# Kernel optimization log

Hardware: AMD Instinct MI355X
Metric: run time of the kernel (lower is better)

The kernel has to match this reference:

```python
import jax, jax.numpy as jnp
import numpy as np
from jax import lax

PART = 224   # PART_IMAGE_SIZE
PAD = 224    # PAD_SIZE
TOPN = 4
IOU_THRESH = 0.25
N_ANCHORS = 1614


def _conv(x, w, b, stride, pad):
    y = lax.conv_general_dilated(x, w, (stride, stride), [(pad, pad), (pad, pad)],
                                 dimension_numbers=('NCHW', 'OIHW', 'NCHW'))
    return y + b[None, :, None, None]


def _iou(box, boxes):
    # box [4], boxes [N,4] as (y0,x0,y1,x1)
    yy0 = jnp.maximum(box[0], boxes[:, 0]); xx0 = jnp.maximum(box[1], boxes[:, 1])
    yy1 = jnp.minimum(box[2], boxes[:, 2]); xx1 = jnp.minimum(box[3], boxes[:, 3])
    inter = jnp.clip(yy1 - yy0, 0.0) * jnp.clip(xx1 - xx0, 0.0)
    a = (box[2] - box[0]) * (box[3] - box[1])
    areas = (boxes[:, 2] - boxes[:, 0]) * (boxes[:, 3] - boxes[:, 1])
    return inter / (a + areas - inter)


def _nms(scores, boxes):
    # hard NMS keeping TOPN boxes; returns indices [TOPN]
    valid = jnp.ones(scores.shape, dtype=bool)
    idxs = []
    for _ in range(TOPN):
        i = jnp.argmax(jnp.where(valid, scores, -jnp.inf))
        idxs.append(i)
        valid = valid & (_iou(boxes[i], boxes) <= IOU_THRESH)
    return jnp.stack(idxs)


def _crop_resize(img, box):
    # img [3,Hp,Wp] padded image, box [4] float; bilinear, align_corners=True,
    # matching F.interpolate(x_pad[:, :, y0:y1, x0:x1], (PART, PART))
    Hp, Wp = img.shape[1], img.shape[2]
    def coords(c0, c1, L):
        t = jnp.arange(PART, dtype=img.dtype) / (PART - 1)
        c = c0 + (c1 - 1.0 - c0) * t          # absolute source coordinate
        cf = jnp.floor(c)
        lo = jnp.clip(cf.astype(jnp.int32), 0, L - 1)
        hi = jnp.clip(lo + 1, 0, L - 1)
        return lo, hi, c - cf
    yl, yh, wy = coords(box[0], box[2], Hp)
    xl, xh, wx = coords(box[1], box[3], Wp)
    g = lambda yi, xi: img[:, yi[:, None], xi[None, :]]   # [3,PART,PART]
    return ((1 - wy)[:, None] * ((1 - wx) * g(yl, xl) + wx * g(yl, xh))
            + wy[:, None] * ((1 - wx) * g(yh, xl) + wx * g(yh, xh)))


def setup_inputs() -> dict:
    key = jax.random.key(0)
    ks = jax.random.split(key, 20)
    x = jax.random.uniform(ks[0], (16, 3, 448, 448), dtype=jnp.float32)
    rpn_feature = jax.random.normal(ks[1], (16, 2048, 14, 14), dtype=jnp.float32)
    # valid boxes inside the padded 896x896 image
    y0 = jax.random.randint(ks[2], (N_ANCHORS,), 0, 560)
    x0 = jax.random.randint(ks[3], (N_ANCHORS,), 0, 560)
    h = jax.random.randint(ks[4], (N_ANCHORS,), 32, 336)
    w = jax.random.randint(ks[5], (N_ANCHORS,), 32, 336)
    anchors = jnp.stack([y0, x0, jnp.minimum(y0 + h, 896), jnp.minimum(x0 + w, 896)], axis=1).astype(jnp.int32)
    s = 0.02
    inp = {
        'x': x, 'rpn_feature': rpn_feature, 'anchors': anchors,
        'w_down1': jax.random.normal(ks[6], (128, 2048, 3, 3), jnp.float32) * s,
        'b_down1': jnp.zeros((128,), jnp.float32),
        'w_down2': jax.random.normal(ks[7], (128, 128, 3, 3), jnp.float32) * s,
        'b_down2': jnp.zeros((128,), jnp.float32),
        'w_down3': jax.random.normal(ks[8], (128, 128, 3, 3), jnp.float32) * s,
        'b_down3': jnp.zeros((128,), jnp.float32),
        'w_tidy1': jax.random.normal(ks[9], (6, 128, 1, 1), jnp.float32) * s,
        'b_tidy1': jnp.zeros((6,), jnp.float32),
        'w_tidy2': jax.random.normal(ks[10], (6, 128, 1, 1), jnp.float32) * s,
        'b_tidy2': jnp.zeros((6,), jnp.float32),
        'w_tidy3': jax.random.normal(ks[11], (9, 128, 1, 1), jnp.float32) * s,
        'b_tidy3': jnp.zeros((9,), jnp.float32),
    }
    return inp


def reference(x, rpn_feature, anchors,
              w_down1, b_down1, w_down2, b_down2, w_down3, b_down3,
              w_tidy1, b_tidy1, w_tidy2, b_tidy2, w_tidy3, b_tidy3):
    B = x.shape[0]
    # ProposalNet
    d1 = jax.nn.relu(_conv(rpn_feature, w_down1, b_down1, 1, 1))   # [B,128,14,14]
    d2 = jax.nn.relu(_conv(d1, w_down2, b_down2, 2, 1))            # [B,128,7,7]
    d3 = jax.nn.relu(_conv(d2, w_down3, b_down3, 2, 1))            # [B,128,4,4]
    t1 = _conv(d1, w_tidy1, b_tidy1, 1, 0).reshape(B, -1)
    t2 = _conv(d2, w_tidy2, b_tidy2, 1, 0).reshape(B, -1)
    t3 = _conv(d3, w_tidy3, b_tidy3, 1, 0).reshape(B, -1)
    rpn_score = jnp.concatenate([t1, t2, t3], axis=1)              # [B, 1614]
    boxes = anchors.astype(x.dtype)                                # [N,4]
    top_n_index = jax.vmap(lambda s: _nms(s, boxes))(rpn_score)    # [B,TOPN]
    top_n_prob = jnp.take_along_axis(rpn_score, top_n_index, axis=1)
    x_pad = jnp.pad(x, ((0, 0), (0, 0), (PAD, PAD), (PAD, PAD)))   # [B,3,896,896]
    sel_boxes = boxes[top_n_index]                                 # [B,TOPN,4]
    part_imgs = jax.vmap(lambda img, bxs: jax.vmap(lambda b: _crop_resize(img, b))(bxs))(x_pad, sel_boxes)
    # part_imgs: [B,TOPN,3,PART,PART]
    return rpn_score, top_n_index, top_n_prob, part_imgs
```

## Files before the change

### kernel.cpp

```cpp
#include <hip/hip_runtime.h>
#include <hip/hip_bf16.h>

#define NB 16
#define NA 1614
#define NBP (NB * 196 * 128)
#define NBP2 (NB * 128 * 49)

typedef __bf16 bf16x8 __attribute__((ext_vector_type(8)));
typedef float f32x4 __attribute__((ext_vector_type(4)));

__device__ __forceinline__ unsigned short f2bf(float v) {
  unsigned u = __float_as_uint(v);
  unsigned r = (u + 0x7FFFu + ((u >> 16) & 1u)) >> 16;
  return (unsigned short)r;
}
__device__ __forceinline__ float bf2f(unsigned short s) {
  return __uint_as_float(((unsigned)s) << 16);
}

__global__ __launch_bounds__(256)
void prep(const float* __restrict__ w, const float* __restrict__ in,
          unsigned short* __restrict__ wTh, unsigned short* __restrict__ wTl,
          unsigned short* __restrict__ aTh, unsigned short* __restrict__ aTl) {
  __shared__ float sbuf[32 * 289];
  const int bid = blockIdx.x;
  if (bid < 1024) {
    const int chunk = bid & 63, b = bid >> 6;
    const float* src = in + ((size_t)b * 2048 + chunk * 32) * 196;
#pragma unroll
    for (int r = 0; r < 7; r++) {
      int e = threadIdx.x + 256 * r;
      if (e < 1568) {
        int ic = e / 49, f = e - ic * 49;
        float4 v = ((const float4*)(src + (size_t)ic * 196))[f];
        float* d = sbuf + ic * 201 + f * 4;
        d[0] = v.x; d[1] = v.y; d[2] = v.z; d[3] = v.w;
      }
    }
    __syncthreads();
    unsigned short* oh = aTh + (size_t)bid * (196 * 32);
    unsigned short* ol = aTl + (size_t)bid * (196 * 32);
#pragma unroll
    for (int r = 0; r < 4; r++) {
      int e = threadIdx.x + 256 * r;
      if (e < 784) {
        int pos = e >> 2, part = e & 3;
        unsigned short hv[8], lv[8];
#pragma unroll
        for (int j = 0; j < 8; j++) {
          float v = sbuf[(part * 8 + j) * 201 + pos];
          unsigned short h = f2bf(v);
          hv[j] = h;
          lv[j] = f2bf(v - bf2f(h));
        }
        ((uint4*)oh)[e] = *(uint4*)hv;
        ((uint4*)ol)[e] = *(uint4*)lv;
      }
    }
  } else {
    const int bid2 = bid - 1024;
    const int ocg = bid2 & 3, ks = (bid2 >> 2) & 3, kcp = bid2 >> 4;
    const int oc0 = ocg * 32;
    const int ic0 = kcp * 128 + ks * 32;
#pragma unroll
    for (int r = 0; r < 9; r++) {
      int f = threadIdx.x + 256 * r;
      int o = f / 72, rem4 = f - o * 72;
      float4 v = *(const float4*)(w + ((size_t)(oc0 + o) * 2048 + ic0) * 9 + rem4 * 4);
      float* d = sbuf + o * 289 + rem4 * 4;
      d[0] = v.x; d[1] = v.y; d[2] = v.z; d[3] = v.w;
    }
    __syncthreads();
#pragma unroll
    for (int r = 0; r < 36; r++) {
      int e = threadIdx.x + 256 * r;
      int tap = e >> 10, rem = e & 1023;
      int o = rem >> 5, ic = rem & 31;
      float v = sbuf[o * 289 + ic * 9 + tap];
      unsigned short h = f2bf(v);
      size_t g2 = ((size_t)(kcp * 36 + tap * 4 + ks) << 12) + oc0 * 32 + rem;
      wTh[g2] = h;
      wTl[g2] = f2bf(v - bf2f(h));
    }
  }
}

#define APL 1360
#define ABUF (4 * APL)

#define LOADB(H, L, T, K)                                                     \
  {                                                                           \
    const size_t o_ = ((size_t)(kc * 36 + (T) * 4 + (K)) << 12) + bln;        \
    const unsigned short* ph_ = wTh + o_;                                     \
    const unsigned short* pq_ = wTl + o_;                                     \
    H[0] = *(const bf16x8*)(ph_);                                             \
    H[1] = *(const bf16x8*)(ph_ + 512);                                       \
    L[0] = *(const bf16x8*)(pq_);                                             \
    L[1] = *(const bf16x8*)(pq_ + 512);                                       \
  }

#define STEP(IT, BUH, BUL, BNH, BNL)                                          \
  {                                                                           \
    const int it_ = (IT);                                                     \
    const int ks_ = it_ / 9, tap_ = it_ - ks_ * 9;                            \
    {             \
      const int ni_ = (it_ < 35) ? it_ + 1 : 35;                              \
      const int nk_ = ni_ / 9, nt_ = ni_ - nk_ * 9;                           \
      LOADB(BNH, BNL, nt_, nk_);                                              \
    }                                                                         \
    if (ks_ < 3) {        \
      if (tap_ == 3 || tap_ == 4) {                                           \
        int e_ = tid + 256 * (tap_ - 3);                                      \
        if (e_ < ne) {                                                        \
          int u_ = pos04 + e_;                                                \
          int pos_ = u_ >> 2, part_ = u_ & 3;                                 \
          int py_ = pos_ / 14, px_ = pos_ - py_ * 14;                         \
          int d_ = (((ks_ + 1) & 1) ? ABUF : 0) + part_ * APL                 \
                   + (py_ + 1 - rowoff) * 136 + (px_ + 1) * 8;                \
          *(uint4*)(sAh + d_) = sgh;                                          \
          *(uint4*)(sAl + d_) = sgl;                                          \
        }                                                                     \
      }                                                                       \
      if (tap_ == 2 || tap_ == 3) {                                           \
        const uint4* gh_ = (const uint4*)(aTh + ((size_t)(b * 64 + kc * 4 + ks_ + 1) * 196) * 32); \
        const uint4* gl_ = (const uint4*)(aTl + ((size_t)(b * 64 + kc * 4 + ks_ + 1) * 196) * 32); \
        int e_ = tid + 256 * (tap_ - 2);                                      \
        if (e_ < ne) { sgh = gh_[pos04 + e_]; sgl = gl_[pos04 + e_]; }        \
      }                                                                       \
    }                                                                         \
    const int t8_ = (tap_ / 3) * 136 + (tap_ - (tap_ / 3) * 3) * 8;           \
    const unsigned short* pah_ = sAh + (ks_ & 1) * ABUF + qoff + t8_;         \
    const unsigned short* pal_ = sAl + (ks_ & 1) * ABUF + qoff + t8_;         \
    bf16x8 afh[7], afl[7];                                                    \
    _Pragma("unroll") for (int mf = 0; mf < 7; mf++) {                        \
      afh[mf] = *(const bf16x8*)(pah_ + abase[mf]);                           \
      afl[mf] = *(const bf16x8*)(pal_ + abase[mf]);                           \
    }                                                                         \
    _Pragma("unroll") for (int mf = 0; mf < 7; mf++)                          \
      _Pragma("unroll") for (int nf = 0; nf < 2; nf++)                        \
        acc[mf][nf] = __builtin_amdgcn_mfma_f32_16x16x32_bf16(afh[mf], BUH[nf], acc[mf][nf], 0, 0, 0); \
    _Pragma("unroll") for (int mf = 0; mf < 7; mf++)                          \
      _Pragma("unroll") for (int nf = 0; nf < 2; nf++)                        \
        acc[mf][nf] = __builtin_amdgcn_mfma_f32_16x16x32_bf16(afl[mf], BUH[nf], acc[mf][nf], 0, 0, 0); \
    _Pragma("unroll") for (int mf = 0; mf < 7; mf++)                          \
      _Pragma("unroll") for (int nf = 0; nf < 2; nf++)                        \
        acc[mf][nf] = __builtin_amdgcn_mfma_f32_16x16x32_bf16(afh[mf], BUL[nf], acc[mf][nf], 0, 0, 0); \
    if (tap_ == 8) __syncthreads();                                           \
  }

__global__ __launch_bounds__(256, 2)
void conv1_mfma(const unsigned short* __restrict__ aTh, const unsigned short* __restrict__ aTl,
                const unsigned short* __restrict__ wTh, const unsigned short* __restrict__ wTl,
                float* __restrict__ p1) {
  const int bid = blockIdx.x;
  const int kc = bid & 15;
  const int b  = (bid >> 4) & 15;
  const int mh = bid >> 8;
  const int tid = threadIdx.x;
  const int wid = tid >> 6, lane = tid & 63;
  const int wn = wid;
  const int q = lane >> 4, ln = lane & 15;

  __shared__ unsigned short sAh[2 * ABUF];
  __shared__ unsigned short sAl[2 * ABUF];

  const int rowoff = 6 * mh;
  const int pos0 = mh ? 98 : 0;
  const int ne   = mh ? 392 : 504;
  const int pos04 = pos0 * 4;

  for (int e = tid; e < 2 * ABUF / 2; e += 256) {
    ((unsigned int*)sAh)[e] = 0u;
    ((unsigned int*)sAl)[e] = 0u;
  }

  int abase[7];
#pragma unroll
  for (int mf = 0; mf < 7; mf++) {
    int row = mh * 112 + mf * 16 + ln;
    int y = row / 14, x = row - y * 14;
    abase[mf] = (row < 196) ? ((y - rowoff) * 136 + x * 8) : 0;
  }
  const int qoff = q * APL;
  const int bln = (wn * 32 + ln) * 32 + q * 8;

  f32x4 acc[7][2];
#pragma unroll
  for (int mf = 0; mf < 7; mf++)
#pragma unroll
    for (int nf = 0; nf < 2; nf++) acc[mf][nf] = (f32x4){0.f, 0.f, 0.f, 0.f};

  uint4 sgh = {}, sgl = {};

  __syncthreads();

  {
    const uint4* gh = (const uint4*)(aTh + ((size_t)(b * 64 + kc * 4) * 196) * 32);
    const uint4* gl = (const uint4*)(aTl + ((size_t)(b * 64 + kc * 4) * 196) * 32);
#pragma unroll
    for (int r = 0; r < 2; r++) {
      int e = tid + 256 * r;
      if (e < ne) {
        int u = pos04 + e;
        int pos = u >> 2, part = u & 3;
        int py = pos / 14, px = pos - py * 14;
        int d = part * APL + (py + 1 - rowoff) * 136 + (px + 1) * 8;
        *(uint4*)(sAh + d) = gh[u];
        *(uint4*)(sAl + d) = gl[u];
      }
    }
  }
  bf16x8 b0h[2], b0l[2], b1h[2], b1l[2];
  LOADB(b0h, b0l, 0, 0);
  __syncthreads();

  for (int it = 0; it < 36; it += 2) {
    STEP(it,     b0h, b0l, b1h, b1l);
    STEP(it + 1, b1h, b1l, b0h, b0l);
  }

  float* pk = p1 + ((size_t)kc * NB + b) * 196 * 128;
#pragma unroll
  for (int mf = 0; mf < 7; mf++) {
    const int row0 = mh * 112 + mf * 16 + q * 4;
#pragma unroll
    for (int nf = 0; nf < 2; nf++) {
      const int oc = wn * 32 + nf * 16 + ln;
#pragma unroll
      for (int r = 0; r < 4; r++) {
        const int row = row0 + r;
        if (row < 196) pk[(size_t)row * 128 + oc] = acc[mf][nf][r];
      }
    }
  }
}

__global__ __launch_bounds__(256)
void conv1_finish_p(const float* __restrict__ p1, const float* __restrict__ bias,
                    float* __restrict__ d1) {
  __shared__ float s[28 * 132];
  const int bid = blockIdx.x;
  const int pt = bid % 7, b = bid / 7;
  const int tid = threadIdx.x;
#pragma unroll
  for (int r = 0; r < 4; r++) {
    int u = tid + 256 * r;
    if (u < 896) {
      int pos = u >> 5, oc4 = u & 31;
      const float* base = p1 + ((size_t)(b * 196 + pt * 28 + pos)) * 128 + oc4 * 4;
      float4 sum = ((const float4*)bias)[oc4];
#pragma unroll
      for (int k = 0; k < 16; k++) {
        float4 v = *(const float4*)(base + (size_t)k * NBP);
        sum.x += v.x; sum.y += v.y; sum.z += v.z; sum.w += v.w;
      }
      sum.x = fmaxf(sum.x, 0.f); sum.y = fmaxf(sum.y, 0.f);
      sum.z = fmaxf(sum.z, 0.f); sum.w = fmaxf(sum.w, 0.f);
      *(float4*)(s + pos * 132 + oc4 * 4) = sum;
    }
  }
  __syncthreads();
#pragma unroll
  for (int r = 0; r < 4; r++) {
    int u = tid + 256 * r;
    if (u < 896) {
      int oc = u / 7, f = u - oc * 7;
      float4 v;
      v.x = s[(f * 4 + 0) * 132 + oc];
      v.y = s[(f * 4 + 1) * 132 + oc];
      v.z = s[(f * 4 + 2) * 132 + oc];
      v.w = s[(f * 4 + 3) * 132 + oc];
      *(float4*)(d1 + ((size_t)b * 128 + oc) * 196 + pt * 28 + f * 4) = v;
    }
  }
}

__global__ void conv2_part(const float* __restrict__ d1, const float* __restrict__ w,
                           float* __restrict__ p2) {
  const int bid = blockIdx.x;
  const int kc = bid & 3, oct = (bid >> 2) & 3, b = bid >> 4;
  const int ic0 = kc * 32, oc0 = oct * 32;
  const int tid = threadIdx.x;
  const int icg = tid >> 6;
  const int ocq = (tid >> 3) & 7;
  const int rw  = tid & 7;

  __shared__ float s_in[32 * 320];
  __shared__ float s_w[32 * 324];

#pragma unroll
  for (int r = 0; r < 32; r++) {
    const int e = tid + 256 * r;
    const int ch = e >> 8, idx = e & 255;
    const int tr = idx >> 4, tc = idx & 15;
    const int iy = tr - 1, ix = tc - 1;
    float v = 0.f;
    if ((unsigned)iy < 14u && (unsigned)ix < 14u)
      v = d1[((size_t)b * 128 + ic0 + ch) * 196 + iy * 14 + ix];
    s_in[ch * 320 + tr * 20 + tc] = v;
  }
#pragma unroll
  for (int r = 0; r < 36; r++) {
    const int e = tid + 256 * r;
    const int oc = e / 288, rem = e - oc * 288;
    const int ch = rem / 9, tap = rem - ch * 9;
    s_w[ch * 324 + tap * 36 + oc] =
        w[(size_t)(oc0 + oc) * 1152 + (size_t)ic0 * 9 + rem];
  }
  __syncthreads();

  float acc[4][7];
#pragma unroll
  for (int oc = 0; oc < 4; oc++)
#pragma unroll
    for (int x = 0; x < 7; x++) acc[oc][x] = 0.f;

  if (rw < 7) {
    for (int ic = 0; ic < 8; ic++) {
      const int ci = icg * 8 + ic;
      const float* irow = s_in + ci * 320;
      const float* wq = s_w + ci * 324 + ocq * 4;
#pragma unroll
      for (int ky = 0; ky < 3; ky++) {
        const float* r = irow + (2 * rw + ky) * 20;
        const float4 f0 = *(const float4*)(r);
        const float4 f1 = *(const float4*)(r + 4);
        const float4 f2 = *(const float4*)(r + 8);
        const float4 f3 = *(const float4*)(r + 12);
        const float ev[8] = {f0.x, f0.z, f1.x, f1.z, f2.x, f2.z, f3.x, f3.z};
        const float od[7] = {f0.y, f0.w, f1.y, f1.w, f2.y, f2.w, f3.y};
        const float4 w0 = *(const float4*)(wq + (ky * 3 + 0) * 36);
        const float4 w1 = *(const float4*)(wq + (ky * 3 + 1) * 36);
        const float4 w2 = *(const float4*)(wq + (ky * 3 + 2) * 36);
        const float w0a[4] = {w0.x, w0.y, w0.z, w0.w};
        const float w1a[4] = {w1.x, w1.y, w1.z, w1.w};
        const float w2a[4] = {w2.x, w2.y, w2.z, w2.w};
#pragma unroll
        for (int oc = 0; oc < 4; oc++) {
          const float a0 = w0a[oc], a1 = w1a[oc], a2 = w2a[oc];
#pragma unroll
          for (int x = 0; x < 7; x++)
            acc[oc][x] = fmaf(a0, ev[x], fmaf(a1, od[x], fmaf(a2, ev[x + 1], acc[oc][x])));
        }
      }
    }
  }
  __syncthreads();

  if (icg > 0 && rw < 7) {
    float* dst = s_w + ((icg - 1) * 56 + ocq * 7 + rw) * 28;
#pragma unroll
    for (int oc = 0; oc < 4; oc++)
#pragma unroll
      for (int x = 0; x < 7; x++) dst[oc * 7 + x] = acc[oc][x];
  }
  __syncthreads();
  if (icg == 0 && rw < 7) {
#pragma unroll
    for (int g = 0; g < 3; g++) {
      const float* src = s_w + (g * 56 + ocq * 7 + rw) * 28;
#pragma unroll
      for (int oc = 0; oc < 4; oc++)
#pragma unroll
        for (int x = 0; x < 7; x++) acc[oc][x] += src[oc * 7 + x];
    }
    float* po = p2 + (((size_t)kc * NB + b) * 128 + oc0 + ocq * 4) * 49 + rw * 7;
#pragma unroll
    for (int oc = 0; oc < 4; oc++)
#pragma unroll
      for (int x = 0; x < 7; x++) po[oc * 49 + x] = acc[oc][x];
  }
}

__global__ void conv3_part(const float* __restrict__ p2, const float* __restrict__ bd2,
                           const float* __restrict__ w, float* __restrict__ p3) {
  const int bid = blockIdx.x;
  const int kc = bid & 1, oct = (bid >> 1) & 7, b = bid >> 4;
  const int ic0 = kc * 64, oc0 = oct * 16;
  const int tid = threadIdx.x;
  const int oc = tid >> 4, p = tid & 15;
  const int y = p >> 2, x = p & 3;

  __shared__ float s_in[64 * 108];
  __shared__ float s_w[64 * 144];

#pragma unroll
  for (int r = 0; r < 21; r++) {
    const int e = tid + 256 * r;
    if (e < 64 * 81) {
      const int ch = e / 81, idx = e - ch * 81;
      const int tr = idx / 9, tc = idx - tr * 9;
      const int iy = tr - 1, ix = tc - 1;
      float v = 0.f;
      if ((unsigned)iy < 7u && (unsigned)ix < 7u) {
        const size_t ii = ((size_t)b * 128 + ic0 + ch) * 49 + iy * 7 + ix;
        v = bd2[ic0 + ch] + p2[ii];
        v += p2[(size_t)NBP2 + ii];
        v += p2[(size_t)2 * NBP2 + ii];
        v += p2[(size_t)3 * NBP2 + ii];
        v = fmaxf(v, 0.f);
      }
      s_in[ch * 108 + tr * 12 + tc] = v;
    }
  }
#pragma unroll
  for (int r = 0; r < 36; r++) {
    const int e = tid + 256 * r;
    const int o = e / 576, rem = e - o * 576;
    const int ch = rem / 9, tap = rem - ch * 9;
    s_w[ch * 144 + tap * 16 + o] =
        w[(size_t)(oc0 + o) * 1152 + (size_t)ic0 * 9 + rem];
  }
  __syncthreads();

  float acc = 0.f;
  for (int ic = 0; ic < 64; ic++) {
    const float* wrow = s_w + ic * 144 + oc;
    const float* irow = s_in + ic * 108 + 2 * y * 12 + 2 * x;
#pragma unroll
    for (int ky = 0; ky < 3; ky++)
#pragma unroll
      for (int kx = 0; kx < 3; kx++)
        acc = fmaf(wrow[(ky * 3 + kx) * 16], irow[ky * 12 + kx], acc);
  }
  p3[(((size_t)kc * NB + b) * 128 + oc0 + oc) * 16 + p] = acc;
}

__global__ __launch_bounds__(256, 1)
void score_nms(const float* __restrict__ d1,
               const float* __restrict__ p2, const float* __restrict__ bd2,
               const float* __restrict__ p3, const float* __restrict__ bd3,
               const float* __restrict__ w1, const float* __restrict__ b1,
               const float* __restrict__ w2, const float* __restrict__ b2,
               const float* __restrict__ w3, const float* __restrict__ b3,
               const int* __restrict__ anchors, float* __restrict__ score,
               float* __restrict__ out_idx, float* __restrict__ out_prob,
               float* __restrict__ sel) {
  __shared__ float s_in[32 * 200];
  __shared__ float s_w[21 * 128];
  __shared__ float s_b[21];
  __shared__ float s_sc[NA];
  __shared__ float s_bx[NA * 4];
  __shared__ float r_s[256];
  __shared__ int r_i[256];
  const int b = blockIdx.x, tid = threadIdx.x;

  for (int i = tid; i < 768; i += 256) s_w[i] = w1[i];
  for (int i = tid; i < 768; i += 256) s_w[768 + i] = w2[i];
  for (int i = tid; i < 1152; i += 256) s_w[1536 + i] = w3[i];
  if (tid < 21) s_b[tid] = (tid < 6) ? b1[tid] : (tid < 12) ? b2[tid - 6] : b3[tid - 12];
  for (int i = tid; i < NA; i += 256) {
    s_bx[i * 4 + 0] = (float)anchors[i * 4 + 0];
    s_bx[i * 4 + 1] = (float)anchors[i * 4 + 1];
    s_bx[i * 4 + 2] = (float)anchors[i * 4 + 2];
    s_bx[i * 4 + 3] = (float)anchors[i * 4 + 3];
  }

  float acc[5] = {0.f, 0.f, 0.f, 0.f, 0.f};
  for (int chunk = 0; chunk < 4; chunk++) {
    __syncthreads();
    const float* src = d1 + ((size_t)b * 128 + chunk * 32) * 196;
#pragma unroll
    for (int r = 0; r < 7; r++) {
      int e = tid + 256 * r;
      if (e < 1568) {
        int ic = e / 49, f = e - ic * 49;
        *(float4*)(s_in + ic * 200 + f * 4) = ((const float4*)(src + (size_t)ic * 196))[f];
      }
    }
    __syncthreads();
#pragma unroll
    for (int k = 0; k < 5; k++) {
      int j = tid + 256 * k;
      if (j < 1176) {
        int oc = j / 196, p = j - oc * 196;
        const float* wr = s_w + oc * 128 + chunk * 32;
        float s = acc[k];
#pragma unroll
        for (int ic = 0; ic < 32; ic++) s = fmaf(wr[ic], s_in[ic * 200 + p], s);
        acc[k] = s;
      }
    }
  }
#pragma unroll
  for (int k = 0; k < 5; k++) {
    int j = tid + 256 * k;
    if (j < 1176) {
      int oc = j / 196;
      float s = acc[k] + s_b[oc];
      s_sc[j] = s;
      score[b * NA + j] = s;
    }
  }

  __syncthreads();
  {
    const size_t base = (size_t)b * 6272;
#pragma unroll
    for (int r = 0; r < 7; r++) {
      int e = tid + 256 * r;
      if (e < 1568) {
        const float4 v0 = *(const float4*)(p2 + base + e * 4);
        const float4 v1 = *(const float4*)(p2 + (size_t)NBP2 + base + e * 4);
        const float4 v2 = *(const float4*)(p2 + (size_t)2 * NBP2 + base + e * 4);
        const float4 v3 = *(const float4*)(p2 + (size_t)3 * NBP2 + base + e * 4);
        const float s0[4] = {v0.x, v0.y, v0.z, v0.w};
        const float s1[4] = {v1.x, v1.y, v1.z, v1.w};
        const float s2[4] = {v2.x, v2.y, v2.z, v2.w};
        const float s3[4] = {v3.x, v3.y, v3.z, v3.w};
        float o[4];
#pragma unroll
        for (int k = 0; k < 4; k++) {
          const int oc = (e * 4 + k) / 49;
          float s = bd2[oc] + s0[k];
          s += s1[k]; s += s2[k]; s += s3[k];
          o[k] = fmaxf(s, 0.f);
        }
        float4 vv; vv.x = o[0]; vv.y = o[1]; vv.z = o[2]; vv.w = o[3];
        *(float4*)(s_in + e * 4) = vv;
      }
    }
  }
  __syncthreads();
#pragma unroll
  for (int k = 0; k < 2; k++) {
    int jj = tid + 256 * k;
    if (jj < 294) {
      int oc = jj / 49, p = jj - oc * 49;
      const float* wr = s_w + 768 + oc * 128;
      float s = s_b[6 + oc];
#pragma unroll 8
      for (int ic = 0; ic < 128; ic++) s = fmaf(wr[ic], s_in[ic * 49 + p], s);
      s_sc[1176 + jj] = s;
      score[b * NA + 1176 + jj] = s;
    }
  }

  __syncthreads();
  {
    const float4* s0 = (const float4*)(p3 + (size_t)b * 2048);
    const float4* s1 = (const float4*)(p3 + 32768 + (size_t)b * 2048);
#pragma unroll
    for (int r = 0; r < 2; r++) {
      int e = tid + 256 * r;
      if (e < 512) {
        float4 a = s0[e], c = s1[e];
        float bb = bd3[e >> 2];
        float4 v;
        v.x = fmaxf(a.x + c.x + bb, 0.f);
        v.y = fmaxf(a.y + c.y + bb, 0.f);
        v.z = fmaxf(a.z + c.z + bb, 0.f);
        v.w = fmaxf(a.w + c.w + bb, 0.f);
        *(float4*)(s_in + e * 4) = v;
      }
    }
  }
  __syncthreads();
  if (tid < 144) {
    int oc = tid >> 4, p = tid & 15;
    const float* wr = s_w + 1536 + oc * 128;
    float s = s_b[12 + oc];
#pragma unroll 8
    for (int ic = 0; ic < 128; ic++) s = fmaf(wr[ic], s_in[ic * 16 + p], s);
    s_sc[1470 + tid] = s;
    score[b * NA + 1470 + tid] = s;
  }
  __syncthreads();

  for (int t = 0; t < 4; t++) {
    float bs = -__builtin_inff();
    int bi = NA;
    for (int i = tid; i < NA; i += 256) {
      float s = s_sc[i];
      if (s > bs || (s == bs && i < bi)) { bs = s; bi = i; }
    }
    r_s[tid] = bs; r_i[tid] = bi;
    __syncthreads();
    for (int off = 128; off > 0; off >>= 1) {
      if (tid < off) {
        float s2 = r_s[tid + off]; int i2 = r_i[tid + off];
        if (s2 > r_s[tid] || (s2 == r_s[tid] && i2 < r_i[tid])) { r_s[tid] = s2; r_i[tid] = i2; }
      }
      __syncthreads();
    }
    const int idx = r_i[0];
    const float by0 = s_bx[idx * 4 + 0], bx0 = s_bx[idx * 4 + 1];
    const float by1 = s_bx[idx * 4 + 2], bx1 = s_bx[idx * 4 + 3];
    if (tid == 0) {
      out_idx[b * 4 + t] = (float)idx;
      out_prob[b * 4 + t] = s_sc[idx];
      sel[(b * 4 + t) * 4 + 0] = by0;
      sel[(b * 4 + t) * 4 + 1] = bx0;
      sel[(b * 4 + t) * 4 + 2] = by1;
      sel[(b * 4 + t) * 4 + 3] = bx1;
    }
    __syncthreads();
    const float a = (by1 - by0) * (bx1 - bx0);
    for (int i = tid; i < NA; i += 256) {
      float cy0 = s_bx[i * 4 + 0], cx0 = s_bx[i * 4 + 1];
      float cy1 = s_bx[i * 4 + 2], cx1 = s_bx[i * 4 + 3];
      float yy0 = fmaxf(by0, cy0), xx0 = fmaxf(bx0, cx0);
      float yy1 = fminf(by1, cy1), xx1 = fminf(bx1, cx1);
      float inter = fmaxf(yy1 - yy0, 0.f) * fmaxf(xx1 - xx0, 0.f);
      float ar = (cy1 - cy0) * (cx1 - cx0);
      float iou = inter / (a + ar - inter);
      if (iou > 0.25f) s_sc[i] = -__builtin_inff();
    }
    __syncthreads();
  }
}

__global__ void crop_kernel(const float* __restrict__ x, const float* __restrict__ sel,
                            float* __restrict__ out) {
  int i4 = blockIdx.x * 256 + threadIdx.x;
  const int total4 = NB * 4 * 3 * 224 * 56;
  if (i4 >= total4) return;
  int px0 = (i4 % 56) * 4;
  int t = i4 / 56;
  int py = t % 224; t /= 224;
  int ch = t % 3;  t /= 3;
  int n  = t % 4;
  int b  = t / 4;

  const float* bx = sel + (b * 4 + n) * 4;
  const float y0 = bx[0], x0 = bx[1], y1 = bx[2], x1 = bx[3];

  float ty = (float)py / 223.0f;
  float cy = y0 + (y1 - 1.0f - y0) * ty;
  float cyf = floorf(cy);
  int ylo = (int)cyf; ylo = ylo < 0 ? 0 : (ylo > 895 ? 895 : ylo);
  int yhi = ylo + 1 > 895 ? 895 : ylo + 1;
  float wy = cy - cyf;

  const float* img = x + ((size_t)b * 3 + ch) * 448 * 448;
  auto g = [&](int yy, int xx) -> float {
    yy -= 224; xx -= 224;
    if ((unsigned)yy < 448u && (unsigned)xx < 448u)
      return img[(size_t)yy * 448 + xx];
    return 0.f;
  };

  float4 res;
  float* rp = &res.x;
#pragma unroll
  for (int k = 0; k < 4; k++) {
    float tx = (float)(px0 + k) / 223.0f;
    float cx = x0 + (x1 - 1.0f - x0) * tx;
    float cxf = floorf(cx);
    int xlo = (int)cxf; xlo = xlo < 0 ? 0 : (xlo > 895 ? 895 : xlo);
    int xhi = xlo + 1 > 895 ? 895 : xlo + 1;
    float wx = cx - cxf;
    float v00 = g(ylo, xlo), v01 = g(ylo, xhi);
    float v10 = g(yhi, xlo), v11 = g(yhi, xhi);
    rp[k] = (1.f - wy) * ((1.f - wx) * v00 + wx * v01) +
            wy * ((1.f - wx) * v10 + wx * v11);
  }
  *(float4*)(out + (size_t)i4 * 4) = res;
}

extern "C" void kernel_launch(void* const* d_in, const int* in_sizes, int n_in,
                              void* d_out, int out_size, void* d_ws, size_t ws_size,
                              hipStream_t stream) {
  const float* x    = (const float*)d_in[0];
  const float* rpn  = (const float*)d_in[1];
  const int*   anc  = (const int*)d_in[2];
  const float* w_d1 = (const float*)d_in[3];
  const float* b_d1 = (const float*)d_in[4];
  const float* w_d2 = (const float*)d_in[5];
  const float* b_d2 = (const float*)d_in[6];
  const float* w_d3 = (const float*)d_in[7];
  const float* b_d3 = (const float*)d_in[8];
  const float* w_t1 = (const float*)d_in[9];
  const float* b_t1 = (const float*)d_in[10];
  const float* w_t2 = (const float*)d_in[11];
  const float* b_t2 = (const float*)d_in[12];
  const float* w_t3 = (const float*)d_in[13];
  const float* b_t3 = (const float*)d_in[14];

  float* out = (float*)d_out;
  float* ws = (float*)d_ws;

  float* d1  = ws;
  float* d2  = d1 + 401408;
  float* d3  = d2 + 100352;
  float* sel = d3 + 32768;
  float* p2  = sel + 256;
  float* p3  = p2 + 401408;
  unsigned short* wTh = (unsigned short*)(p3 + 65536);
  unsigned short* wTl = wTh + 2359296;
  unsigned short* aTh = wTl + 2359296;
  unsigned short* aTl = aTh + 6422528;

  float* score    = out;
  float* out_idx  = out + 25824;
  float* out_prob = out + 25888;
  float* parts    = out + 25952;
  float* p1       = parts;

  prep<<<dim3(1280), dim3(256), 0, stream>>>(w_d1, rpn, wTh, wTl, aTh, aTl);
  conv1_mfma<<<dim3(512), dim3(256), 0, stream>>>(aTh, aTl, wTh, wTl, p1);
  conv1_finish_p<<<dim3(112), dim3(256), 0, stream>>>(p1, b_d1, d1);
  conv2_part<<<dim3(256), dim3(256), 0, stream>>>(d1, w_d2, p2);
  conv3_part<<<dim3(256), dim3(256), 0, stream>>>(p2, b_d2, w_d3, p3);
  score_nms<<<dim3(16), dim3(256), 0, stream>>>(d1, p2, b_d2, p3, b_d3, w_t1, b_t1, w_t2, b_t2,
                                                w_t3, b_t3, anc, score, out_idx, out_prob, sel);
  crop_kernel<<<dim3(9408), dim3(256), 0, stream>>>(x, sel, parts);
}
```

Baseline: 277.5 us.

## Split conv1 finish into more blocks and drop conv2 in-block channel reduction

conv1_finish_p now handles 7 positions per block across 448 blocks instead of 28 positions across 112, so more CUs share the 16-way partial-sum reduction. Its output stores become scalar rather than float4. conv2_part now gives each thread one output channel across all 32 input channels, rather than 4 channels over a quarter of the inputs followed by a shared-memory cross-group reduction. This removes two syncthreads and the reduction pass, but each thread runs a longer serial loop with fewer weight reuses per input load.

```diff
diff --git a/kernel.cpp b/kernel.cpp
--- a/kernel.cpp
+++ b/kernel.cpp
@@ -238,39 +238,30 @@
 __global__ __launch_bounds__(256)
 void conv1_finish_p(const float* __restrict__ p1, const float* __restrict__ bias,
                     float* __restrict__ d1) {
-  __shared__ float s[28 * 132];
+  __shared__ float s[7 * 132];
   const int bid = blockIdx.x;
-  const int pt = bid % 7, b = bid / 7;
+  const int pt = bid % 28, b = bid / 28;
   const int tid = threadIdx.x;
+  if (tid < 224) {
+    int pos = tid >> 5, oc4 = tid & 31;
+    const float* base = p1 + ((size_t)(b * 196 + pt * 7 + pos)) * 128 + oc4 * 4;
+    float4 sum = ((const float4*)bias)[oc4];
+#pragma unroll
+    for (int k = 0; k < 16; k++) {
+      float4 v = *(const float4*)(base + (size_t)k * NBP);
+      sum.x += v.x; sum.y += v.y; sum.z += v.z; sum.w += v.w;
+    }
+    sum.x = fmaxf(sum.x, 0.f); sum.y = fmaxf(sum.y, 0.f);
+    sum.z = fmaxf(sum.z, 0.f); sum.w = fmaxf(sum.w, 0.f);
+    *(float4*)(s + pos * 132 + oc4 * 4) = sum;
+  }
+  __syncthreads();
 #pragma unroll
   for (int r = 0; r < 4; r++) {
-    int u = tid + 256 * r;
-    if (u < 896) {
-      int pos = u >> 5, oc4 = u & 31;
-      const float* base = p1 + ((size_t)(b * 196 + pt * 28 + pos)) * 128 + oc4 * 4;
-      float4 sum = ((const float4*)bias)[oc4];
-#pragma unroll
-      for (int k = 0; k < 16; k++) {
-        float4 v = *(const float4*)(base + (size_t)k * NBP);
-        sum.x += v.x; sum.y += v.y; sum.z += v.z; sum.w += v.w;
-      }
-      sum.x = fmaxf(sum.x, 0.f); sum.y = fmaxf(sum.y, 0.f);
-      sum.z = fmaxf(sum.z, 0.f); sum.w = fmaxf(sum.w, 0.f);
-      *(float4*)(s + pos * 132 + oc4 * 4) = sum;
-    }
-  }
-  __syncthreads();
-#pragma unroll
-  for (int r = 0; r < 4; r++) {
-    int u = tid + 256 * r;
-    if (u < 896) {
-      int oc = u / 7, f = u - oc * 7;
-      float4 v;
-      v.x = s[(f * 4 + 0) * 132 + oc];
-      v.y = s[(f * 4 + 1) * 132 + oc];
-      v.z = s[(f * 4 + 2) * 132 + oc];
-      v.w = s[(f * 4 + 3) * 132 + oc];
-      *(float4*)(d1 + ((size_t)b * 128 + oc) * 196 + pt * 28 + f * 4) = v;
+    int e = tid + 256 * r;
+    if (e < 896) {
+      int oc = e / 7, f = e - oc * 7;
+      d1[((size_t)b * 128 + oc) * 196 + pt * 7 + f] = s[f * 132 + oc];
     }
   }
 }
@@ -281,9 +272,7 @@
   const int kc = bid & 3, oct = (bid >> 2) & 3, b = bid >> 4;
   const int ic0 = kc * 32, oc0 = oct * 32;
   const int tid = threadIdx.x;
-  const int icg = tid >> 6;
-  const int ocq = (tid >> 3) & 7;
-  const int rw  = tid & 7;
+  const int ocl = tid >> 3, rw = tid & 7;
 
   __shared__ float s_in[32 * 320];
   __shared__ float s_w[32 * 324];
@@ -309,17 +298,11 @@
   }
   __syncthreads();
 
-  float acc[4][7];
-#pragma unroll
-  for (int oc = 0; oc < 4; oc++)
-#pragma unroll
-    for (int x = 0; x < 7; x++) acc[oc][x] = 0.f;
-
   if (rw < 7) {
-    for (int ic = 0; ic < 8; ic++) {
-      const int ci = icg * 8 + ic;
-      const float* irow = s_in + ci * 320;
-      const float* wq = s_w + ci * 324 + ocq * 4;
+    float acc[7] = {};
+    for (int ic = 0; ic < 32; ic++) {
+      const float* wrow = s_w + ic * 324 + ocl;
+      const float* irow = s_in + ic * 320;
 #pragma unroll
       for (int ky = 0; ky < 3; ky++) {
         const float* r = irow + (2 * rw + ky) * 20;
@@ -329,46 +312,17 @@
         const float4 f3 = *(const float4*)(r + 12);
         const float ev[8] = {f0.x, f0.z, f1.x, f1.z, f2.x, f2.z, f3.x, f3.z};
         const float od[7] = {f0.y, f0.w, f1.y, f1.w, f2.y, f2.w, f3.y};
-        const float4 w0 = *(const float4*)(wq + (ky * 3 + 0) * 36);
-        const float4 w1 = *(const float4*)(wq + (ky * 3 + 1) * 36);
-        const float4 w2 = *(const float4*)(wq + (ky * 3 + 2) * 36);
-        const float w0a[4] = {w0.x, w0.y, w0.z, w0.w};
-        const float w1a[4] = {w1.x, w1.y, w1.z, w1.w};
-        const float w2a[4] = {w2.x, w2.y, w2.z, w2.w};
-#pragma unroll
-        for (int oc = 0; oc < 4; oc++) {
-          const float a0 = w0a[oc], a1 = w1a[oc], a2 = w2a[oc];
-#pragma unroll
-          for (int x = 0; x < 7; x++)
-            acc[oc][x] = fmaf(a0, ev[x], fmaf(a1, od[x], fmaf(a2, ev[x + 1], acc[oc][x])));
-        }
-      }
-    }
-  }
-  __syncthreads();
-
-  if (icg > 0 && rw < 7) {
-    float* dst = s_w + ((icg - 1) * 56 + ocq * 7 + rw) * 28;
-#pragma unroll
-    for (int oc = 0; oc < 4; oc++)
-#pragma unroll
-      for (int x = 0; x < 7; x++) dst[oc * 7 + x] = acc[oc][x];
-  }
-  __syncthreads();
-  if (icg == 0 && rw < 7) {
-#pragma unroll
-    for (int g = 0; g < 3; g++) {
-      const float* src = s_w + (g * 56 + ocq * 7 + rw) * 28;
-#pragma unroll
-      for (int oc = 0; oc < 4; oc++)
-#pragma unroll
-        for (int x = 0; x < 7; x++) acc[oc][x] += src[oc * 7 + x];
-    }
-    float* po = p2 + (((size_t)kc * NB + b) * 128 + oc0 + ocq * 4) * 49 + rw * 7;
-#pragma unroll
-    for (int oc = 0; oc < 4; oc++)
-#pragma unroll
-      for (int x = 0; x < 7; x++) po[oc * 49 + x] = acc[oc][x];
+        const float w0 = wrow[(ky * 3 + 0) * 36];
+        const float w1 = wrow[(ky * 3 + 1) * 36];
+        const float w2 = wrow[(ky * 3 + 2) * 36];
+#pragma unroll
+        for (int x = 0; x < 7; x++)
+          acc[x] = fmaf(w0, ev[x], fmaf(w1, od[x], fmaf(w2, ev[x + 1], acc[x])));
+      }
+    }
+    float* po = p2 + (((size_t)kc * NB + b) * 128 + oc0 + ocl) * 49 + rw * 7;
+#pragma unroll
+    for (int x = 0; x < 7; x++) po[x] = acc[x];
   }
 }
 
@@ -699,7 +653,7 @@
 
   prep<<<dim3(1280), dim3(256), 0, stream>>>(w_d1, rpn, wTh, wTl, aTh, aTl);
   conv1_mfma<<<dim3(512), dim3(256), 0, stream>>>(aTh, aTl, wTh, wTl, p1);
-  conv1_finish_p<<<dim3(112), dim3(256), 0, stream>>>(p1, b_d1, d1);
+  conv1_finish_p<<<dim3(448), dim3(256), 0, stream>>>(p1, b_d1, d1);
   conv2_part<<<dim3(256), dim3(256), 0, stream>>>(d1, w_d2, p2);
   conv3_part<<<dim3(256), dim3(256), 0, stream>>>(p2, b_d2, w_d3, p3);
   score_nms<<<dim3(16), dim3(256), 0, stream>>>(d1, p2, b_d2, p3, b_d3, w_t1, b_t1, w_t2, b_t2,
```

Result: no change. 279.2 us, median of 2 (+0.6%).
